# Kernel optimization log

Measured on AMD Instinct MI355X. Metric: run time of the kernel, lower is better.

## Reference

```python
import jax, jax.numpy as jnp
import numpy as np
from jax import lax

# dims: T steps, B batch, V vocab, E embed, H hidden, N cache slots, DK key dim, DV value dim
T, B, V, E, H, N, DK, DV = 64, 32, 32000, 512, 512, 512, 256, 512


def setup_inputs() -> dict:
    key = jax.random.key(0)
    ks = jax.random.split(key, 12)
    rn = lambda i, shape, scale: jax.random.normal(ks[i], shape, jnp.float32) * scale
    return {
        "tokens": jax.random.randint(ks[0], (T, B), 0, V),
        "emb": rn(1, (V, E), 0.02),
        "Wq": rn(2, (E, DK), E ** -0.5),
        "Wk": rn(3, (E, DK), E ** -0.5),
        "Wv": rn(4, (H, DV), H ** -0.5),
        "Wh": rn(5, (E + DV, H), (E + DV) ** -0.5),
        "bh": jnp.zeros((H,), jnp.float32),
        "Wout": rn(6, (H, V), H ** -0.5),
        "bout": jnp.zeros((V,), jnp.float32),
        "keys0": rn(7, (N, DK), 0.02),
        "values0": rn(8, (N, DV), 0.02),
        "k": 8,
    }


def reference(tokens, emb, Wq, Wk, Wv, Wh, bh, Wout, bout, keys0, values0, k):
    scale = 1.0 / jnp.sqrt(jnp.float32(DK))

    def step(carry, tok_t):
        keys, vals, ptr = carry
        x = emb[tok_t]                                  # [B, E] embedding gather
        q = x @ Wq                                      # [B, DK]
        scores = (q @ keys.T) * scale                   # [B, N]
        top_s, top_i = lax.top_k(scores, k)             # [B, k]
        w = jax.nn.softmax(top_s, axis=-1)              # [B, k]
        v_sel = vals[top_i]                             # [B, k, DV] irregular gather
        retrieved = jnp.einsum('bk,bkd->bd', w, v_sel)  # [B, DV]
        h = jnp.tanh(jnp.concatenate([x, retrieved], axis=-1) @ Wh + bh)  # [B, H]
        # circular-pointer cache write (batch-pooled key/value)
        new_key = jnp.mean(x @ Wk, axis=0)              # [DK]
        new_val = jnp.mean(h @ Wv, axis=0)              # [DV]
        keys = lax.dynamic_update_slice(keys, new_key[None, :], (ptr, 0))
        vals = lax.dynamic_update_slice(vals, new_val[None, :], (ptr, 0))
        ptr = (ptr + 1) % N
        return (keys, vals, ptr), h

    init = (keys0, values0, jnp.int32(0))
    _, hiddens = lax.scan(step, init, tokens)           # [T, B, H]
    logits = hiddens @ Wout + bout                      # [T, B, V]
    return logits
```

## Files before the change

kernel.cpp:

```cpp
#include <hip/hip_runtime.h>

typedef _Float16 half_t;
typedef _Float16 half8 __attribute__((ext_vector_type(8)));
typedef float f32x4 __attribute__((ext_vector_type(4)));


__device__ __forceinline__ void gload_lds16(const void* g, void* l) {
  __builtin_amdgcn_global_load_lds((const __attribute__((address_space(1))) void*)g,
                                   (__attribute__((address_space(3))) void*)l, 16, 0, 0);
}

__device__ __forceinline__ void prepTile(int pid, const float* __restrict__ Wout,
                                         half_t* __restrict__ WoutT,
                                         const float* __restrict__ Wh,
                                         half_t* __restrict__ W1T,
                                         half_t* __restrict__ W2T,
                                         char* smem) {
  half_t (*tile)[68] = (half_t(*)[68])smem;
  if (pid < 4000) {
    int n0 = (pid % 500) * 64, k0 = (pid / 500) * 64;
    for (int p = 0; p < 4; p++) {
      int id = p * 256 + threadIdx.x;
      int k = id >> 4, nq = id & 15;
      float4 v = *(const float4*)&Wout[(size_t)(k0 + k) * 32000 + n0 + nq * 4];
      tile[nq * 4 + 0][k] = (half_t)v.x; tile[nq * 4 + 1][k] = (half_t)v.y;
      tile[nq * 4 + 2][k] = (half_t)v.z; tile[nq * 4 + 3][k] = (half_t)v.w;
    }
    __syncthreads();
    for (int p = 0; p < 2; p++) {
      int id = p * 256 + threadIdx.x;
      int n = id >> 3, kc = id & 7;
      half8 h = *(const half8*)&tile[n][kc * 8];
      *(half8*)&WoutT[(size_t)(n0 + n) * 512 + k0 + kc * 8] = h;
    }
  } else {
    int id2 = pid - 4000;
    int n0 = (id2 & 7) * 64, k0 = (id2 >> 3) * 64;
    for (int p = 0; p < 16; p++) {
      int id = p * 256 + threadIdx.x;
      int kk = id >> 6, nn = id & 63;
      tile[nn][kk] = (half_t)Wh[(size_t)(k0 + kk) * 512 + n0 + nn];
    }
    __syncthreads();
    half_t* out = (k0 < 512) ? W1T : W2T;
    int kb = k0 & 511;
    for (int p = 0; p < 16; p++) {
      int id = p * 256 + threadIdx.x;
      int nn = id >> 6, kk = id & 63;
      out[(size_t)(n0 + nn) * 512 + kb + kk] = tile[nn][kk];
    }
  }
}

__global__ __launch_bounds__(256) void kGE(const int* __restrict__ tok,
                                           const float* __restrict__ emb,
                                           const float* __restrict__ Wq,
                                           const float* __restrict__ Wk,
                                           double* __restrict__ Qd,
                                           float* __restrict__ Q32,
                                           half_t* __restrict__ Xh,
                                           double* __restrict__ NKd,
                                           float* __restrict__ NKf,
                                           const float* __restrict__ Wout,
                                           half_t* __restrict__ WoutT,
                                           const float* __restrict__ Wh,
                                           half_t* __restrict__ W1T,
                                           half_t* __restrict__ W2T,
                                           int* __restrict__ DEP,
                                           int* __restrict__ bars) {
  __shared__ __align__(16) char smem[8704];
  int bid = blockIdx.x, tid = threadIdx.x;
  if (bid >= 1024) {
    if (bid < 5152) prepTile(bid - 1024, Wout, WoutT, Wh, W1T, W2T, smem);
    else { if (tid < 64) DEP[tid] = 0; bars[tid] = 0; }
    return;
  }
  if (bid < 512) {
    float (*xs)[512] = (float(*)[512])smem;
    int r0 = bid * 4;
    for (int rr = 0; rr < 4; rr++) {
      int row = r0 + rr;
      const float* src = emb + (size_t)tok[row] * 512;
      float v0 = src[tid], v1 = src[tid + 256];
      xs[rr][tid] = v0; xs[rr][tid + 256] = v1;
      Xh[(size_t)row * 512 + tid] = (half_t)v0;
      Xh[(size_t)row * 512 + tid + 256] = (half_t)v1;
    }
    __syncthreads();
    int d = tid;
    double a0 = 0, a1 = 0, a2 = 0, a3 = 0;
    #pragma unroll 4
    for (int i = 0; i < 512; i++) {
      double w = (double)Wq[(size_t)i * 256 + d];
      a0 += (double)xs[0][i] * w; a1 += (double)xs[1][i] * w;
      a2 += (double)xs[2][i] * w; a3 += (double)xs[3][i] * w;
    }
    Qd[(size_t)(r0 + 0) * 256 + d] = a0; Qd[(size_t)(r0 + 1) * 256 + d] = a1;
    Qd[(size_t)(r0 + 2) * 256 + d] = a2; Qd[(size_t)(r0 + 3) * 256 + d] = a3;
    Q32[(size_t)(r0 + 0) * 256 + d] = (float)a0; Q32[(size_t)(r0 + 1) * 256 + d] = (float)a1;
    Q32[(size_t)(r0 + 2) * 256 + d] = (float)a2; Q32[(size_t)(r0 + 3) * 256 + d] = (float)a3;
  } else {
    double* xm = (double*)smem;
    int bid2 = bid - 512, t = bid2 >> 3, ch = bid2 & 7;
    int c = tid;
    double s0 = 0.0, s1 = 0.0;
    for (int b = 0; b < 32; b++) {
      const float* src = emb + (size_t)tok[t * 32 + b] * 512;
      s0 += (double)src[c]; s1 += (double)src[c + 256];
    }
    xm[c] = s0 * (1.0 / 32.0);
    xm[c + 256] = s1 * (1.0 / 32.0);
    __syncthreads();
    if (tid < 32) {
      int d = ch * 32 + tid;
      double a = 0;
      #pragma unroll 4
      for (int i = 0; i < 512; i++) a += xm[i] * (double)Wk[(size_t)i * 256 + d];
      NKd[(size_t)t * 256 + d] = a;
      NKf[(size_t)t * 256 + d] = (float)a;
    }
  }
}

__global__ __launch_bounds__(256) void kS(const float* __restrict__ Q32,
                                          const float* __restrict__ keys0,
                                          const float* __restrict__ NKf,
                                          float* __restrict__ S) {
  __shared__ float As[32][68];
  __shared__ float Bs[32][68];
  int b = blockIdx.x, tid = threadIdx.x;
  int m0 = (b & 31) * 64, n0 = (b >> 5) * 64;
  int tx = tid & 15, ty = tid >> 4;
  float acc[4][4];
  #pragma unroll
  for (int i = 0; i < 4; i++)
    #pragma unroll
    for (int j = 0; j < 4; j++) acc[i][j] = 0.f;
  for (int kc = 0; kc < 256; kc += 32) {
    __syncthreads();
    #pragma unroll
    for (int p = 0; p < 8; p++) {
      int idx = p * 256 + tid;
      int k = idx & 31, m = idx >> 5;
      As[k][m] = Q32[(size_t)(m0 + m) * 256 + kc + k];
      int n = n0 + m;
      Bs[k][m] = (n < 512) ? keys0[(size_t)n * 256 + kc + k]
                           : NKf[(size_t)(n - 512) * 256 + kc + k];
    }
    __syncthreads();
    #pragma unroll
    for (int k = 0; k < 32; k++) {
      float4 a = *(const float4*)&As[k][ty * 4];
      float4 bb = *(const float4*)&Bs[k][tx * 4];
      acc[0][0] += a.x * bb.x; acc[0][1] += a.x * bb.y; acc[0][2] += a.x * bb.z; acc[0][3] += a.x * bb.w;
      acc[1][0] += a.y * bb.x; acc[1][1] += a.y * bb.y; acc[1][2] += a.y * bb.z; acc[1][3] += a.y * bb.w;
      acc[2][0] += a.z * bb.x; acc[2][1] += a.z * bb.y; acc[2][2] += a.z * bb.z; acc[2][3] += a.z * bb.w;
      acc[3][0] += a.w * bb.x; acc[3][1] += a.w * bb.y; acc[3][2] += a.w * bb.z; acc[3][3] += a.w * bb.w;
    }
  }
  #pragma unroll
  for (int i = 0; i < 4; i++) {
    float4 o = {acc[i][0], acc[i][1], acc[i][2], acc[i][3]};
    *(float4*)&S[(size_t)(m0 + ty * 4 + i) * 576 + n0 + tx * 4] = o;
  }
}

__global__ __launch_bounds__(256) void kTR(const float* __restrict__ S,
                                           const double* __restrict__ Qd,
                                           const double* __restrict__ NKd,
                                           const float* __restrict__ keys0,
                                           const float* __restrict__ vals0,
                                           float* __restrict__ WSo,
                                           int* __restrict__ ISo,
                                           half_t* __restrict__ R16,
                                           int* __restrict__ DEP) {
  __shared__ float wls[4][8];
  __shared__ int ils[4][8];
  __shared__ int depf;
  int bid = blockIdx.x, tid = threadIdx.x;
  if (tid == 0) depf = 0;
  __syncthreads();
  int r0b = bid * 4;
  int wv = tid >> 6, lane = tid & 63;
  int row = r0b + wv;
  int t = row >> 5;
  const float* Srow = S + (size_t)row * 576;
  float v[8];
  #pragma unroll
  for (int j = 0; j < 8; j++) v[j] = Srow[j * 64 + lane];
  if (lane < t) v[0] = Srow[512 + lane];
  int ci[12];
  #pragma unroll
  for (int it = 0; it < 12; it++) {
    float bv = -1e30f; int bi = 0x7fffffff;
    #pragma unroll
    for (int j = 0; j < 8; j++) {
      int ii = j * 64 + lane;
      if (v[j] > bv || (v[j] == bv && ii < bi)) { bv = v[j]; bi = ii; }
    }
    #pragma unroll
    for (int s = 32; s > 0; s >>= 1) {
      float ov = __shfl_xor(bv, s, 64);
      int oi = __shfl_xor(bi, s, 64);
      if (ov > bv || (ov == bv && oi < bi)) { bv = ov; bi = oi; }
    }
    ci[it] = bi;
    #pragma unroll
    for (int j = 0; j < 8; j++)
      if (j * 64 + lane == bi) v[j] = -1e30f;
  }
  const double* qrow = Qd + (size_t)row * 256 + lane * 4;
  double q0 = qrow[0], q1 = qrow[1], q2 = qrow[2], q3 = qrow[3];
  double dv[12];
  #pragma unroll
  for (int c = 0; c < 12; c++) {
    int idx = ci[c];
    double p;
    if (idx < t) {
      const double* kr = NKd + (size_t)idx * 256 + lane * 4;
      p = q0 * kr[0] + q1 * kr[1] + q2 * kr[2] + q3 * kr[3];
    } else {
      const float* kr = keys0 + (size_t)idx * 256 + lane * 4;
      p = q0 * (double)kr[0] + q1 * (double)kr[1] + q2 * (double)kr[2] + q3 * (double)kr[3];
    }
    #pragma unroll
    for (int s = 32; s > 0; s >>= 1) p += __shfl_xor(p, s, 64);
    dv[c] = p * 0.0625;
  }
  double tv[8]; int ti[8];
  #pragma unroll
  for (int it = 0; it < 8; it++) {
    double bv = -1e300; int bi = 0x7fffffff;
    #pragma unroll
    for (int c = 0; c < 12; c++)
      if (dv[c] > bv || (dv[c] == bv && ci[c] < bi)) { bv = dv[c]; bi = ci[c]; }
    tv[it] = bv; ti[it] = bi;
    #pragma unroll
    for (int c = 0; c < 12; c++)
      if (ci[c] == bi) dv[c] = -1e300;
  }
  if (lane == 0) {
    double m = tv[0], ev[8], Z = 0;
    #pragma unroll
    for (int i2 = 0; i2 < 8; i2++) { ev[i2] = exp(tv[i2] - m); Z += ev[i2]; }
    double inv = 1.0 / Z;
    int dep = 0;
    #pragma unroll
    for (int i2 = 0; i2 < 8; i2++) {
      float w = (float)(ev[i2] * inv);
      WSo[(size_t)row * 8 + i2] = w;
      ISo[(size_t)row * 8 + i2] = ti[i2];
      wls[wv][i2] = w; ils[wv][i2] = ti[i2];
      if (ti[i2] < t) dep = 1;
    }
    if (dep) atomicOr(&depf, 1);
  }
  __syncthreads();
  if (tid == 0 && depf) atomicOr(&DEP[t], 1);
  for (int rr = 0; rr < 4; rr++) {
    float a0 = 0.f, a1 = 0.f;
    #pragma unroll
    for (int k2 = 0; k2 < 8; k2++) {
      const float* src = vals0 + (size_t)ils[rr][k2] * 512;
      a0 += wls[rr][k2] * src[tid];
      a1 += wls[rr][k2] * src[tid + 256];
    }
    R16[(size_t)(r0b + rr) * 512 + tid] = (half_t)a0;
    R16[(size_t)(r0b + rr) * 512 + tid + 256] = (half_t)a1;
  }
}

__device__ __forceinline__ void gbar(int* bars, int id, int nwg) {
  __syncthreads();
  if (threadIdx.x == 0) {
    __hip_atomic_fetch_add(&bars[id], 1, __ATOMIC_ACQ_REL, __HIP_MEMORY_SCOPE_AGENT);
    while (__hip_atomic_load(&bars[id], __ATOMIC_ACQUIRE, __HIP_MEMORY_SCOPE_AGENT) < nwg)
      __builtin_amdgcn_s_sleep(4);
  }
  __syncthreads();
}

__global__ __launch_bounds__(256) void kH(const half_t* __restrict__ Xh,
                                          const half_t* __restrict__ R16,
                                          const half_t* __restrict__ W1T,
                                          const half_t* __restrict__ W2T,
                                          const float* __restrict__ bh,
                                          const float* __restrict__ Wv,
                                          float* __restrict__ XH,
                                          half_t* __restrict__ HH,
                                          float* __restrict__ HM,
                                          float* __restrict__ NV,
                                          int* __restrict__ bars) {
  __shared__ half_t lA[3][64 * 32];
  __shared__ half_t lB[3][64 * 32];
  __shared__ float hmld[512];
  int b = blockIdx.x;
  int m0 = (b >> 3) * 64, n0 = (b & 7) * 64;
  int tid = threadIdx.x, wid = tid >> 6, lane = tid & 63;
  int wm = wid >> 1, wn = wid & 1;
  f32x4 acc[2][2];
  #pragma unroll
  for (int i = 0; i < 2; i++)
    #pragma unroll
    for (int j = 0; j < 2; j++) acc[i][j] = (f32x4){0.f, 0.f, 0.f, 0.f};
  int rA = lane >> 2;
  int cswz = ((lane & 3) ^ ((lane >> 3) & 3)) * 8;
  int koffs = (((lane >> 4) ^ ((lane >> 1) & 3))) * 8;
  auto issue = [&](int j, int buf) {
    const half_t* Ap = (j < 16) ? Xh : R16;
    const half_t* Bp = (j < 16) ? W1T : W2T;
    int kk = j & 15;
    gload_lds16(Ap + ((size_t)(m0 + wid * 16 + rA) * 512 + kk * 32 + cswz), (void*)(&lA[buf][wid * 512]));
    gload_lds16(Bp + ((size_t)(n0 + wid * 16 + rA) * 512 + kk * 32 + cswz), (void*)(&lB[buf][wid * 512]));
  };
  issue(0, 0); issue(1, 1);
  for (int kt = 0; kt < 32; kt++) {
    if (kt < 31) asm volatile("s_waitcnt vmcnt(2)\n\ts_barrier" ::: "memory");
    else         asm volatile("s_waitcnt vmcnt(0)\n\ts_barrier" ::: "memory");
    int cur = kt % 3;
    half8 af[2], bf[2];
    #pragma unroll
    for (int mf = 0; mf < 2; mf++)
      af[mf] = *(const half8*)&lA[cur][(wm * 32 + mf * 16 + (lane & 15)) * 32 + koffs];
    #pragma unroll
    for (int nf = 0; nf < 2; nf++)
      bf[nf] = *(const half8*)&lB[cur][(wn * 32 + nf * 16 + (lane & 15)) * 32 + koffs];
    if (kt < 30) issue(kt + 2, (kt + 2) % 3);
    #pragma unroll
    for (int mf = 0; mf < 2; mf++)
      #pragma unroll
      for (int nf = 0; nf < 2; nf++)
        acc[mf][nf] = __builtin_amdgcn_mfma_f32_16x16x32_f16(af[mf], bf[nf], acc[mf][nf], 0, 0, 0);
    if (kt == 15) {
      #pragma unroll
      for (int nf = 0; nf < 2; nf++) {
        int col = n0 + wn * 32 + nf * 16 + (lane & 15);
        float bv = bh[col];
        #pragma unroll
        for (int mf = 0; mf < 2; mf++) {
          int rbase = m0 + wm * 32 + mf * 16 + (lane >> 4) * 4;
          #pragma unroll
          for (int r = 0; r < 4; r++)
            XH[(size_t)(rbase + r) * 512 + col] = acc[mf][nf][r] + bv;
        }
      }
    }
  }
  #pragma unroll
  for (int nf = 0; nf < 2; nf++) {
    int col = n0 + wn * 32 + nf * 16 + (lane & 15);
    float bv = bh[col];
    float cs = 0.f;
    #pragma unroll
    for (int mf = 0; mf < 2; mf++) {
      int rbase = m0 + wm * 32 + mf * 16 + (lane >> 4) * 4;
      #pragma unroll
      for (int r = 0; r < 4; r++) {
        float v = tanhf(acc[mf][nf][r] + bv);
        HH[(size_t)(rbase + r) * 512 + col] = (half_t)v;
        cs += v;
      }
    }
    cs += __shfl_xor(cs, 16, 64);
    cs += __shfl_xor(cs, 32, 64);
    if ((lane >> 4) == 0) {
      int t = (m0 >> 5) + wm;
      HM[(size_t)t * 512 + col] = cs * (1.f / 32.f);
    }
  }
  gbar(bars, 0, 256);
  int t2 = b >> 2, ch = b & 3;
  hmld[tid] = HM[(size_t)t2 * 512 + tid];
  hmld[tid + 256] = HM[(size_t)t2 * 512 + tid + 256];
  __syncthreads();
  if (tid < 128) {
    int col = ch * 128 + tid;
    float a = 0.f;
    #pragma unroll 4
    for (int i = 0; i < 512; i++) a += hmld[i] * Wv[(size_t)i * 512 + col];
    NV[(size_t)t2 * 512 + col] = a;
  }
}

__global__ __launch_bounds__(256) void kFixup(const int* __restrict__ DEP,
                                              int* __restrict__ bars,
                                              const float* __restrict__ XHm,
                                              const float* __restrict__ Wh,
                                              const float* __restrict__ Wv,
                                              const float* __restrict__ vals0,
                                              const float* __restrict__ WSo,
                                              const int* __restrict__ ISo,
                                              float* __restrict__ NV,
                                              float* __restrict__ RETR,
                                              float* __restrict__ HB,
                                              half_t* __restrict__ HHm) {
  __shared__ float rl[512];
  __shared__ float hm2[512];
  int w = blockIdx.x;
  int barid = 0;
  for (int t = 0; t < 64; t++) {
    if (DEP[t] == 0) continue;
    {
      int b = w >> 1, hf = w & 1;
      int c = hf * 256 + threadIdx.x;
      int row = t * 32 + b;
      float acc = 0.f;
      #pragma unroll
      for (int k2 = 0; k2 < 8; k2++) {
        int idx = ISo[(size_t)row * 8 + k2];
        float wv2 = WSo[(size_t)row * 8 + k2];
        const float* src = (idx < t) ? (NV + (size_t)idx * 512) : (vals0 + (size_t)idx * 512);
        acc += wv2 * src[c];
      }
      RETR[(size_t)b * 512 + c] = acc;
    }
    gbar(bars, barid++, 64);
    if (w < 32) {
      int b = w;
      rl[threadIdx.x] = RETR[(size_t)b * 512 + threadIdx.x];
      rl[threadIdx.x + 256] = RETR[(size_t)b * 512 + threadIdx.x + 256];
      __syncthreads();
      int row = t * 32 + b;
      for (int cc = 0; cc < 2; cc++) {
        int col = cc * 256 + threadIdx.x;
        float acc = 0.f;
        #pragma unroll 4
        for (int i = 0; i < 512; i++) acc += rl[i] * Wh[(size_t)(512 + i) * 512 + col];
        float h = tanhf(XHm[(size_t)row * 512 + col] + acc);
        HB[(size_t)b * 512 + col] = h;
        HHm[(size_t)row * 512 + col] = (half_t)h;
      }
    }
    gbar(bars, barid++, 64);
    if (w == 0) {
      for (int j = threadIdx.x; j < 512; j += 256) {
        float s = 0.f;
        for (int b = 0; b < 32; b++) s += HB[(size_t)b * 512 + j];
        hm2[j] = s * (1.f / 32.f);
      }
      __syncthreads();
      for (int v = threadIdx.x; v < 512; v += 256) {
        float a = 0.f;
        #pragma unroll 4
        for (int i = 0; i < 512; i++) a += hm2[i] * Wv[(size_t)i * 512 + v];
        NV[(size_t)t * 512 + v] = a;
      }
    }
    gbar(bars, barid++, 64);
  }
}

__global__ __launch_bounds__(256) void kLogits(const half_t* __restrict__ A,
                                               const half_t* __restrict__ Bm,
                                               const float* __restrict__ bout,
                                               float* __restrict__ C) {
  __shared__ __align__(16) char smem[49152];
  half_t* lAb = (half_t*)smem;
  half_t* lBb = (half_t*)(smem + 24576);
  int lin = blockIdx.y * 250 + blockIdx.x;
  int swz = (lin & 7) * 500 + (lin >> 3);
  int m0 = (swz & 15) * 128;
  int n0 = (swz >> 4) * 128;
  int tid = threadIdx.x, wid = tid >> 6, lane = tid & 63;
  int wm = wid >> 1, wn = wid & 1;
  f32x4 acc[4][4];
  #pragma unroll
  for (int a2 = 0; a2 < 4; a2++)
    #pragma unroll
    for (int b2 = 0; b2 < 4; b2++) acc[a2][b2] = (f32x4){0.f, 0.f, 0.f, 0.f};
  int rA = lane >> 2;
  int cswz = ((lane & 3) ^ ((lane >> 3) & 3)) * 8;
  int koffs = (((lane >> 4) ^ ((lane >> 1) & 3))) * 8;
  auto issue = [&](int j, int buf) {
    #pragma unroll
    for (int i2 = 0; i2 < 2; i2++) {
      int blk = wid * 2 + i2;
      gload_lds16(A + ((size_t)(m0 + blk * 16 + rA) * 512 + j * 32 + cswz), (void*)(lAb + buf * 4096 + blk * 512));
      gload_lds16(Bm + ((size_t)(n0 + blk * 16 + rA) * 512 + j * 32 + cswz), (void*)(lBb + buf * 4096 + blk * 512));
    }
  };
  issue(0, 0); issue(1, 1);
  for (int kt = 0; kt < 16; kt++) {
    if (kt < 15) asm volatile("s_waitcnt vmcnt(4)\n\ts_barrier" ::: "memory");
    else         asm volatile("s_waitcnt vmcnt(0)\n\ts_barrier" ::: "memory");
    int cur = kt % 3;
    half8 af[4], bf[4];
    #pragma unroll
    for (int mf = 0; mf < 4; mf++)
      af[mf] = *(const half8*)(lAb + cur * 4096 + (wm * 64 + mf * 16 + (lane & 15)) * 32 + koffs);
    #pragma unroll
    for (int nf = 0; nf < 4; nf++)
      bf[nf] = *(const half8*)(lBb + cur * 4096 + (wn * 64 + nf * 16 + (lane & 15)) * 32 + koffs);
    if (kt < 14) issue(kt + 2, (kt + 2) % 3);
    #pragma unroll
    for (int mf = 0; mf < 4; mf++)
      #pragma unroll
      for (int nf = 0; nf < 4; nf++)
        acc[mf][nf] = __builtin_amdgcn_mfma_f32_16x16x32_f16(af[mf], bf[nf], acc[mf][nf], 0, 0, 0);
  }
  float (*cst)[128] = (float(*)[128])smem;
  #pragma unroll
  for (int half = 0; half < 2; half++) {
    __syncthreads();
    if (wm == half) {
      #pragma unroll
      for (int nf = 0; nf < 4; nf++) {
        int col = wn * 64 + nf * 16 + (lane & 15);
        #pragma unroll
        for (int mf = 0; mf < 4; mf++) {
          int rr = mf * 16 + (lane >> 4) * 4;
          #pragma unroll
          for (int r = 0; r < 4; r++)
            cst[rr + r][col] = acc[mf][nf][r];
        }
      }
    }
    __syncthreads();
    #pragma unroll
    for (int p = 0; p < 8; p++) {
      int idx = p * 256 + tid;
      int rr = idx >> 5, cc = idx & 31;
      float4 v = *(float4*)&cst[rr][cc * 4];
      const float4 bv = *(const float4*)&bout[n0 + cc * 4];
      v.x += bv.x; v.y += bv.y; v.z += bv.z; v.w += bv.w;
      *(float4*)&C[(size_t)(m0 + half * 64 + rr) * 32000 + n0 + cc * 4] = v;
    }
  }
}

extern "C" void kernel_launch(void* const* d_in, const int* in_sizes, int n_in,
                              void* d_out, int out_size, void* d_ws, size_t ws_size,
                              hipStream_t stream) {
  (void)in_sizes; (void)n_in; (void)out_size; (void)ws_size;
  const int*   tok   = (const int*)d_in[0];
  const float* emb   = (const float*)d_in[1];
  const float* Wq    = (const float*)d_in[2];
  const float* Wk    = (const float*)d_in[3];
  const float* Wv    = (const float*)d_in[4];
  const float* Wh    = (const float*)d_in[5];
  const float* bh    = (const float*)d_in[6];
  const float* Wout  = (const float*)d_in[7];
  const float* bout  = (const float*)d_in[8];
  const float* keys0 = (const float*)d_in[9];
  const float* vals0 = (const float*)d_in[10];
  float* Cout = (float*)d_out;

  char* ws = (char*)d_ws;
  size_t off = 0;
  auto alloc = [&](size_t bytes) -> char* {
    char* p = ws + off;
    off += (bytes + 255) & ~(size_t)255;
    return p;
  };
  half_t* WoutT = (half_t*)alloc(32768000);
  half_t* W1T   = (half_t*)alloc(524288);
  half_t* W2T   = (half_t*)alloc(524288);
  half_t* Xh    = (half_t*)alloc(2097152);
  double* Qd    = (double*)alloc(4194304);
  float*  Q32   = (float*) alloc(2097152);
  double* NKd   = (double*)alloc(131072);
  float*  NKf   = (float*) alloc(65536);
  float*  Sb    = (float*) alloc(4718592);
  float*  XH    = (float*) alloc(4194304);
  float*  WSb   = (float*) alloc(65536);
  int*    ISb   = (int*)   alloc(65536);
  float*  NV    = (float*) alloc(131072);
  half_t* R16   = (half_t*)alloc(2097152);
  half_t* HH    = (half_t*)alloc(2097152);
  float*  HM    = (float*) alloc(131072);
  float*  RETR  = (float*) alloc(65536);
  float*  HB    = (float*) alloc(65536);
  int*    DEP   = (int*)   alloc(256);
  int*    bars  = (int*)   alloc(1024);

  kGE<<<5153, 256, 0, stream>>>(tok, emb, Wq, Wk, Qd, Q32, Xh, NKd, NKf,
                                Wout, WoutT, Wh, W1T, W2T, DEP, bars);
  kS<<<288, 256, 0, stream>>>(Q32, keys0, NKf, Sb);
  kTR<<<512, 256, 0, stream>>>(Sb, Qd, NKd, keys0, vals0, WSb, ISb, R16, DEP);
  kH<<<256, 256, 0, stream>>>(Xh, R16, W1T, W2T, bh, Wv, XH, HH, HM, NV, bars);
  kFixup<<<64, 256, 0, stream>>>(DEP, bars + 16, XH, Wh, Wv, vals0, WSb, ISb, NV, RETR, HB, HH);
  kLogits<<<dim3(250, 16), 256, 0, stream>>>(HH, WoutT, bout, Cout);
}
```

Before: 335.5 us.

## Enlarge logits GEMM tiles to 256x256 with 512 threads and double-buffered LDS

Rewrites the output-projection GEMM to compute 256x256 tiles per 512-thread block, staging 64-wide K chunks with an XOR-swizzled LDS layout and double buffering. MFMA issue is raised in priority with s_setprio, and the epilogue writes accumulators plus bias directly to global memory without LDS staging. The aim is to cut global operand traffic and barrier count per FLOP. The direct epilogue stores are less vectorized than the previous float4 path, and the large LDS footprint limits occupancy.

Result: no change. 331.2 us (-1.3%).

```diff
diff --git a/kernel.cpp b/kernel.cpp
--- a/kernel.cpp
+++ b/kernel.cpp
@@ -450,82 +450,86 @@
   }
 }
 
-__global__ __launch_bounds__(256) void kLogits(const half_t* __restrict__ A,
-                                               const half_t* __restrict__ Bm,
-                                               const float* __restrict__ bout,
-                                               float* __restrict__ C) {
-  __shared__ __align__(16) char smem[49152];
-  half_t* lAb = (half_t*)smem;
-  half_t* lBb = (half_t*)(smem + 24576);
-  int lin = blockIdx.y * 250 + blockIdx.x;
-  int swz = (lin & 7) * 500 + (lin >> 3);
-  int m0 = (swz & 15) * 128;
-  int n0 = (swz >> 4) * 128;
+__global__ __launch_bounds__(512, 2) void kLogits(const half_t* __restrict__ A,
+                                                  const half_t* __restrict__ Bm,
+                                                  const float* __restrict__ bout,
+                                                  float* __restrict__ C) {
+  __shared__ __align__(16) char smem[131072];
+  int lin = blockIdx.x;
+  int g = (lin & 7) * 125 + (lin >> 3);
+  int ntile = g >> 3, mtile = g & 7;
+  int m0 = mtile * 256, n0 = ntile * 256;
   int tid = threadIdx.x, wid = tid >> 6, lane = tid & 63;
-  int wm = wid >> 1, wn = wid & 1;
-  f32x4 acc[4][4];
-  #pragma unroll
-  for (int a2 = 0; a2 < 4; a2++)
-    #pragma unroll
-    for (int b2 = 0; b2 < 4; b2++) acc[a2][b2] = (f32x4){0.f, 0.f, 0.f, 0.f};
-  int rA = lane >> 2;
-  int cswz = ((lane & 3) ^ ((lane >> 3) & 3)) * 8;
-  int koffs = (((lane >> 4) ^ ((lane >> 1) & 3))) * 8;
-  auto issue = [&](int j, int buf) {
-    #pragma unroll
-    for (int i2 = 0; i2 < 2; i2++) {
-      int blk = wid * 2 + i2;
-      gload_lds16(A + ((size_t)(m0 + blk * 16 + rA) * 512 + j * 32 + cswz), (void*)(lAb + buf * 4096 + blk * 512));
-      gload_lds16(Bm + ((size_t)(n0 + blk * 16 + rA) * 512 + j * 32 + cswz), (void*)(lBb + buf * 4096 + blk * 512));
+  int wm = wid >> 2, wn = wid & 3;
+  int srow = tid >> 3, sslot = tid & 7;
+  f32x4 acc[8][4];
+  #pragma unroll
+  for (int i = 0; i < 8; i++)
+    #pragma unroll
+    for (int j = 0; j < 4; j++) acc[i][j] = (f32x4){0.f, 0.f, 0.f, 0.f};
+  auto issue = [&](int kt, int h) {
+    int b = kt & 1;
+    char* base = (h < 2) ? (smem + b * 32768 + h * 16384)
+                         : (smem + 65536 + b * 32768 + (h - 2) * 16384);
+    const half_t* gb = (h < 2) ? (A + (size_t)(m0 + h * 128) * 512)
+                               : (Bm + (size_t)(n0 + (h - 2) * 128) * 512);
+    #pragma unroll
+    for (int j = 0; j < 2; j++) {
+      int row = srow + j * 64;
+      int koff = kt * 64 + ((sslot ^ (row & 7)) << 3);
+      gload_lds16(gb + (size_t)row * 512 + koff, base + j * 8192 + wid * 1024);
     }
   };
-  issue(0, 0); issue(1, 1);
-  for (int kt = 0; kt < 16; kt++) {
-    if (kt < 15) asm volatile("s_waitcnt vmcnt(4)\n\ts_barrier" ::: "memory");
-    else         asm volatile("s_waitcnt vmcnt(0)\n\ts_barrier" ::: "memory");
-    int cur = kt % 3;
-    half8 af[4], bf[4];
-    #pragma unroll
-    for (int mf = 0; mf < 4; mf++)
-      af[mf] = *(const half8*)(lAb + cur * 4096 + (wm * 64 + mf * 16 + (lane & 15)) * 32 + koffs);
-    #pragma unroll
-    for (int nf = 0; nf < 4; nf++)
-      bf[nf] = *(const half8*)(lBb + cur * 4096 + (wn * 64 + nf * 16 + (lane & 15)) * 32 + koffs);
-    if (kt < 14) issue(kt + 2, (kt + 2) % 3);
-    #pragma unroll
-    for (int mf = 0; mf < 4; mf++)
-      #pragma unroll
-      for (int nf = 0; nf < 4; nf++)
-        acc[mf][nf] = __builtin_amdgcn_mfma_f32_16x16x32_f16(af[mf], bf[nf], acc[mf][nf], 0, 0, 0);
-  }
-  float (*cst)[128] = (float(*)[128])smem;
-  #pragma unroll
-  for (int half = 0; half < 2; half++) {
-    __syncthreads();
-    if (wm == half) {
-      #pragma unroll
-      for (int nf = 0; nf < 4; nf++) {
-        int col = wn * 64 + nf * 16 + (lane & 15);
+  issue(0, 0); issue(0, 1); issue(0, 2); issue(0, 3);
+  for (int kt = 0; kt < 8; kt++) {
+    char* Ab = smem + (kt & 1) * 32768 + wm * 16384;
+    char* Bb = smem + 65536 + (kt & 1) * 32768 + (wn >> 1) * 16384;
+    #pragma unroll
+    for (int p = 0; p < 4; p++) {
+      if (p == 0) asm volatile("s_waitcnt vmcnt(0)" ::: "memory");
+      asm volatile("s_barrier" ::: "memory");
+      if (kt < 7) issue(kt + 1, p);
+      int qm = p >> 1, qn = p & 1;
+      half8 af[4][2], bf[2][2];
+      #pragma unroll
+      for (int fm = 0; fm < 4; fm++)
         #pragma unroll
-        for (int mf = 0; mf < 4; mf++) {
-          int rr = mf * 16 + (lane >> 4) * 4;
+        for (int s = 0; s < 2; s++) {
+          int rl = qm * 64 + fm * 16 + (lane & 15);
+          int slot = s * 4 + (lane >> 4);
+          af[fm][s] = *(const half8*)(Ab + rl * 128 + ((slot ^ (rl & 7)) << 4));
+        }
+      #pragma unroll
+      for (int fn = 0; fn < 2; fn++)
+        #pragma unroll
+        for (int s = 0; s < 2; s++) {
+          int rl = (wn & 1) * 64 + qn * 32 + fn * 16 + (lane & 15);
+          int slot = s * 4 + (lane >> 4);
+          bf[fn][s] = *(const half8*)(Bb + rl * 128 + ((slot ^ (rl & 7)) << 4));
+        }
+      __builtin_amdgcn_s_setprio(1);
+      #pragma unroll
+      for (int s = 0; s < 2; s++)
+        #pragma unroll
+        for (int fm = 0; fm < 4; fm++)
           #pragma unroll
-          for (int r = 0; r < 4; r++)
-            cst[rr + r][col] = acc[mf][nf][r];
-        }
-      }
-    }
-    __syncthreads();
-    #pragma unroll
-    for (int p = 0; p < 8; p++) {
-      int idx = p * 256 + tid;
-      int rr = idx >> 5, cc = idx & 31;
-      float4 v = *(float4*)&cst[rr][cc * 4];
-      const float4 bv = *(const float4*)&bout[n0 + cc * 4];
-      v.x += bv.x; v.y += bv.y; v.z += bv.z; v.w += bv.w;
-      *(float4*)&C[(size_t)(m0 + half * 64 + rr) * 32000 + n0 + cc * 4] = v;
-    }
-  }
+          for (int fn = 0; fn < 2; fn++)
+            acc[qm * 4 + fm][qn * 2 + fn] = __builtin_amdgcn_mfma_f32_16x16x32_f16(
+                af[fm][s], bf[fn][s], acc[qm * 4 + fm][qn * 2 + fn], 0, 0, 0);
+      __builtin_amdgcn_s_setprio(0);
+    }
+  }
+  #pragma unroll
+  for (int mf = 0; mf < 8; mf++)
+    #pragma unroll
+    for (int nf = 0; nf < 4; nf++) {
+      int col = n0 + wn * 64 + nf * 16 + (lane & 15);
+      float bv = bout[col];
+      int rbase = m0 + wm * 128 + mf * 16 + (lane >> 4) * 4;
+      #pragma unroll
+      for (int r = 0; r < 4; r++)
+        C[(size_t)(rbase + r) * 32000 + col] = acc[mf][nf][r] + bv;
+    }
 }
 
 extern "C" void kernel_launch(void* const* d_in, const int* in_sizes, int n_in,
@@ -579,5 +583,5 @@
   kTR<<<512, 256, 0, stream>>>(Sb, Qd, NKd, keys0, vals0, WSb, ISb, R16, DEP);
   kH<<<256, 256, 0, stream>>>(Xh, R16, W1T, W2T, bh, Wv, XH, HH, HM, NV, bars);
   kFixup<<<64, 256, 0, stream>>>(DEP, bars + 16, XH, Wh, Wv, vals0, WSb, ISb, NV, RETR, HB, HH);
-  kLogits<<<dim3(250, 16), 256, 0, stream>>>(HH, WoutT, bout, Cout);
-}
+  kLogits<<<1000, 512, 0, stream>>>(HH, WoutT, bout, Cout);
+}
```

## Retile logits GEMM to 128x256 blocks with 512 threads and direct epilogue

Applied to the files above, without the earlier changes.

The logits GEMM moves from 128x128 tiles with 4 waves to 128x256 tiles with 8 waves, using a 1D grid with a new swizzle. It goes from a three-stage to a two-stage LDS buffer with split A/B prefetch issue, adds s_setprio around the MFMA block, and removes the swizzled LDS layout. The epilogue now writes accumulators straight to global memory with bias instead of staging through LDS for coalesced float4 stores. The aim is more reuse per block and less epilogue overhead. The trade-offs are uncoalesced strided stores to a large output, possible LDS bank conflicts without the swizzle, and less latency hiding from the shallower pipeline.

After: 328.8 us. 2.0% less time.

```diff
diff --git a/kernel.cpp b/kernel.cpp
--- a/kernel.cpp
+++ b/kernel.cpp
@@ -450,80 +450,66 @@
   }
 }
 
-__global__ __launch_bounds__(256) void kLogits(const half_t* __restrict__ A,
-                                               const half_t* __restrict__ Bm,
-                                               const float* __restrict__ bout,
-                                               float* __restrict__ C) {
+__global__ __launch_bounds__(512, 4) void kLogits(const half_t* __restrict__ A,
+                                                  const half_t* __restrict__ Bm,
+                                                  const float* __restrict__ bout,
+                                                  float* __restrict__ C) {
   __shared__ __align__(16) char smem[49152];
-  half_t* lAb = (half_t*)smem;
-  half_t* lBb = (half_t*)(smem + 24576);
-  int lin = blockIdx.y * 250 + blockIdx.x;
-  int swz = (lin & 7) * 500 + (lin >> 3);
-  int m0 = (swz & 15) * 128;
-  int n0 = (swz >> 4) * 128;
+  int lin = blockIdx.x;
+  int g = (lin & 7) * 250 + (lin >> 3);
+  int mtile = g & 15, ntile = g >> 4;
+  int m0 = mtile * 128, n0 = ntile * 256;
   int tid = threadIdx.x, wid = tid >> 6, lane = tid & 63;
-  int wm = wid >> 1, wn = wid & 1;
+  int wm = wid >> 2, wn = wid & 3;
+  int srow = tid >> 2, ssl = tid & 3;
   f32x4 acc[4][4];
   #pragma unroll
-  for (int a2 = 0; a2 < 4; a2++)
-    #pragma unroll
-    for (int b2 = 0; b2 < 4; b2++) acc[a2][b2] = (f32x4){0.f, 0.f, 0.f, 0.f};
-  int rA = lane >> 2;
-  int cswz = ((lane & 3) ^ ((lane >> 3) & 3)) * 8;
-  int koffs = (((lane >> 4) ^ ((lane >> 1) & 3))) * 8;
-  auto issue = [&](int j, int buf) {
-    #pragma unroll
-    for (int i2 = 0; i2 < 2; i2++) {
-      int blk = wid * 2 + i2;
-      gload_lds16(A + ((size_t)(m0 + blk * 16 + rA) * 512 + j * 32 + cswz), (void*)(lAb + buf * 4096 + blk * 512));
-      gload_lds16(Bm + ((size_t)(n0 + blk * 16 + rA) * 512 + j * 32 + cswz), (void*)(lBb + buf * 4096 + blk * 512));
-    }
+  for (int i = 0; i < 4; i++)
+    #pragma unroll
+    for (int j = 0; j < 4; j++) acc[i][j] = (f32x4){0.f, 0.f, 0.f, 0.f};
+  auto issueA = [&](int kt) {
+    gload_lds16(A + (size_t)(m0 + srow) * 512 + kt * 32 + ssl * 8,
+                smem + (kt & 1) * 8192 + tid * 16);
   };
-  issue(0, 0); issue(1, 1);
+  auto issueB = [&](int kt) {
+    #pragma unroll
+    for (int j = 0; j < 2; j++)
+      gload_lds16(Bm + (size_t)(n0 + j * 128 + srow) * 512 + kt * 32 + ssl * 8,
+                  smem + 16384 + (kt & 1) * 16384 + j * 8192 + tid * 16);
+  };
+  issueA(0); issueB(0);
   for (int kt = 0; kt < 16; kt++) {
-    if (kt < 15) asm volatile("s_waitcnt vmcnt(4)\n\ts_barrier" ::: "memory");
-    else         asm volatile("s_waitcnt vmcnt(0)\n\ts_barrier" ::: "memory");
-    int cur = kt % 3;
+    asm volatile("s_waitcnt vmcnt(0)\n\ts_barrier" ::: "memory");
+    if (kt < 15) issueA(kt + 1);
+    char* Ab = smem + (kt & 1) * 8192;
+    char* Bb = smem + 16384 + (kt & 1) * 16384;
+    int ko = (lane >> 4) * 16;
     half8 af[4], bf[4];
     #pragma unroll
     for (int mf = 0; mf < 4; mf++)
-      af[mf] = *(const half8*)(lAb + cur * 4096 + (wm * 64 + mf * 16 + (lane & 15)) * 32 + koffs);
+      af[mf] = *(const half8*)(Ab + (wm * 64 + mf * 16 + (lane & 15)) * 64 + ko);
     #pragma unroll
     for (int nf = 0; nf < 4; nf++)
-      bf[nf] = *(const half8*)(lBb + cur * 4096 + (wn * 64 + nf * 16 + (lane & 15)) * 32 + koffs);
-    if (kt < 14) issue(kt + 2, (kt + 2) % 3);
+      bf[nf] = *(const half8*)(Bb + (wn * 64 + nf * 16 + (lane & 15)) * 64 + ko);
+    __builtin_amdgcn_s_setprio(1);
     #pragma unroll
     for (int mf = 0; mf < 4; mf++)
       #pragma unroll
       for (int nf = 0; nf < 4; nf++)
         acc[mf][nf] = __builtin_amdgcn_mfma_f32_16x16x32_f16(af[mf], bf[nf], acc[mf][nf], 0, 0, 0);
-  }
-  float (*cst)[128] = (float(*)[128])smem;
-  #pragma unroll
-  for (int half = 0; half < 2; half++) {
-    __syncthreads();
-    if (wm == half) {
+    __builtin_amdgcn_s_setprio(0);
+    if (kt < 15) issueB(kt + 1);
+  }
+  #pragma unroll
+  for (int nf = 0; nf < 4; nf++) {
+    int col = n0 + wn * 64 + nf * 16 + (lane & 15);
+    float bv = bout[col];
+    #pragma unroll
+    for (int mf = 0; mf < 4; mf++) {
+      int rbase = m0 + wm * 64 + mf * 16 + (lane >> 4) * 4;
       #pragma unroll
-      for (int nf = 0; nf < 4; nf++) {
-        int col = wn * 64 + nf * 16 + (lane & 15);
-        #pragma unroll
-        for (int mf = 0; mf < 4; mf++) {
-          int rr = mf * 16 + (lane >> 4) * 4;
-          #pragma unroll
-          for (int r = 0; r < 4; r++)
-            cst[rr + r][col] = acc[mf][nf][r];
-        }
-      }
-    }
-    __syncthreads();
-    #pragma unroll
-    for (int p = 0; p < 8; p++) {
-      int idx = p * 256 + tid;
-      int rr = idx >> 5, cc = idx & 31;
-      float4 v = *(float4*)&cst[rr][cc * 4];
-      const float4 bv = *(const float4*)&bout[n0 + cc * 4];
-      v.x += bv.x; v.y += bv.y; v.z += bv.z; v.w += bv.w;
-      *(float4*)&C[(size_t)(m0 + half * 64 + rr) * 32000 + n0 + cc * 4] = v;
+      for (int r = 0; r < 4; r++)
+        C[(size_t)(rbase + r) * 32000 + col] = acc[mf][nf][r] + bv;
     }
   }
 }
@@ -579,5 +565,5 @@
   kTR<<<512, 256, 0, stream>>>(Sb, Qd, NKd, keys0, vals0, WSb, ISb, R16, DEP);
   kH<<<256, 256, 0, stream>>>(Xh, R16, W1T, W2T, bh, Wv, XH, HH, HM, NV, bars);
   kFixup<<<64, 256, 0, stream>>>(DEP, bars + 16, XH, Wh, Wv, vals0, WSb, ISb, NV, RETR, HB, HH);
-  kLogits<<<dim3(250, 16), 256, 0, stream>>>(HH, WoutT, bout, Cout);
-}
+  kLogits<<<2000, 512, 0, stream>>>(HH, WoutT, bout, Cout);
+}
```
